# Kernel optimization log

Measured on AMD Instinct MI355X. Metric: run time of the kernel, lower is better.

Reference implementation:

```python
import jax, jax.numpy as jnp
import numpy as np
from jax import lax

DS = 4  # downsample_factor

def setup_inputs() -> dict:
    key = jax.random.key(0)
    ks = jax.random.split(key, 7)
    B, C, H, W = 4, 256, 256, 256
    Cq = C // 16  # reduction=16
    return {
        "x":  jax.random.normal(ks[0], (B, C, H, W), dtype=jnp.float32),
        "Wq": jax.random.normal(ks[1], (Cq, C), dtype=jnp.float32) * 0.05,
        "bq": jax.random.normal(ks[2], (Cq,), dtype=jnp.float32) * 0.05,
        "Wk": jax.random.normal(ks[3], (Cq, C), dtype=jnp.float32) * 0.05,
        "bk": jax.random.normal(ks[4], (Cq,), dtype=jnp.float32) * 0.05,
        "Wv": jax.random.normal(ks[5], (C, C), dtype=jnp.float32) * 0.05,
        "bv": jax.random.normal(ks[6], (C,), dtype=jnp.float32) * 0.05,
    }

def reference(x, Wq, bq, Wk, bk, Wv, bv):
    B, C, H, W = x.shape
    # MaxPool2d(kernel=DS, stride=DS)
    xd = lax.reduce_window(x, -jnp.inf, lax.max,
                           (1, 1, DS, DS), (1, 1, DS, DS), 'VALID')
    h, w = xd.shape[2], xd.shape[3]
    N = h * w
    # 1x1 convs == channel-wise linear maps
    q = jnp.einsum('oc,bchw->bohw', Wq, xd) + bq[None, :, None, None]
    k = jnp.einsum('oc,bchw->bohw', Wk, xd) + bk[None, :, None, None]
    v = jnp.einsum('oc,bchw->bohw', Wv, xd) + bv[None, :, None, None]
    query = q.reshape(B, -1, N).transpose(0, 2, 1)   # [B, N, Cq]
    key_  = k.reshape(B, -1, N)                      # [B, Cq, N]
    value = v.reshape(B, C, N).transpose(0, 2, 1)    # [B, N, C]
    att = jnp.einsum('bnc,bcm->bnm', query, key_)    # [B, N, N]
    # global-mean threshold masking (zeros, not -inf, per original)
    att = jnp.where(att < att.mean(), 0.0, att)
    att = jax.nn.softmax(att, axis=-1)
    out = jnp.einsum('bnm,bmc->bnc', att, value)     # [B, N, C]
    out = out.transpose(0, 2, 1).reshape(B, C, h, w)
    # bilinear upsample, align_corners=False (half-pixel centers)
    out = jax.image.resize(out, (B, C, H, W), method='bilinear')
    return out + x
```

## Files before the change

### kernel.cpp

```cpp
#include <hip/hip_runtime.h>
#include <hip/hip_bf16.h>
#include <cmath>
#include <cstdint>
#include <cstddef>

typedef unsigned short u16;
typedef __attribute__((ext_vector_type(8))) __bf16 bf16x8;
typedef __attribute__((ext_vector_type(4))) float f32x4;
typedef __attribute__((ext_vector_type(8))) unsigned short us8;
typedef __attribute__((ext_vector_type(4))) unsigned short us4;

static const size_t OFF_ODS   = 0;
static const size_t OFF_QT    = 16777216;
static const size_t OFF_KT    = 17825792;
static const size_t OFF_VT    = 18874368;
static const size_t OFF_SPART = 27262976;
static const size_t OFF_MEAN  = 27295744;

__device__ __forceinline__ void gl2lds16(const void* gsrc, void* ldst) {
  __builtin_amdgcn_global_load_lds(
      (const __attribute__((address_space(1))) unsigned int*)gsrc,
      (__attribute__((address_space(3))) unsigned int*)ldst, 16, 0, 0);
}

__global__ __launch_bounds__(512) void k_front(const float* __restrict__ x,
                                               const float* __restrict__ Wq, const float* __restrict__ bq,
                                               const float* __restrict__ Wk, const float* __restrict__ bk,
                                               const float* __restrict__ Wv, const float* __restrict__ bv,
                                               float* __restrict__ qT, float* __restrict__ kT,
                                               u16* __restrict__ vT, float* __restrict__ Spart) {
  __shared__ float smem[17408];
  float (*xs)[64] = reinterpret_cast<float(*)[64]>(smem);
  float (*part)[64][33] = reinterpret_cast<float(*)[64][33]>(smem);
  float (*red)[32] = reinterpret_cast<float(*)[32]>(smem + 16896);
  const int b = blockIdx.x >> 6, yo = blockIdx.x & 63;
  const int n0 = yo * 64;
  const int tid = threadIdx.x;

  {
    const float* src = x + (size_t)b * 16777216u + (size_t)(4 * yo) * 256u;
#pragma unroll
    for (int i = 0; i < 32; ++i) {
      int u = i * 512 + tid;
      int c = u >> 6, xo = u & 63;
      const float* p0 = src + (size_t)c * 65536u + xo * 4;
      float m = -1e30f;
#pragma unroll
      for (int r = 0; r < 4; ++r) {
        float4 v4 = *reinterpret_cast<const float4*>(p0 + r * 256);
        m = fmaxf(m, fmaxf(fmaxf(v4.x, v4.y), fmaxf(v4.z, v4.w)));
      }
      xs[c][xo] = m;
    }
  }
  __syncthreads();

  {
    const int ci = tid >> 4, ni = tid & 15;
    float vacc[8][4];
#pragma unroll
    for (int j = 0; j < 8; ++j) { vacc[j][0]=0.f; vacc[j][1]=0.f; vacc[j][2]=0.f; vacc[j][3]=0.f; }
    for (int cc4 = 0; cc4 < 64; ++cc4) {
      float4 xv0 = *reinterpret_cast<const float4*>(&xs[cc4*4+0][ni*4]);
      float4 xv1 = *reinterpret_cast<const float4*>(&xs[cc4*4+1][ni*4]);
      float4 xv2 = *reinterpret_cast<const float4*>(&xs[cc4*4+2][ni*4]);
      float4 xv3 = *reinterpret_cast<const float4*>(&xs[cc4*4+3][ni*4]);
#pragma unroll
      for (int j = 0; j < 8; ++j) {
        float4 wv = *reinterpret_cast<const float4*>(&Wv[(size_t)(ci*8 + j) * 256u + cc4*4]);
        vacc[j][0] = fmaf(wv.x, xv0.x, fmaf(wv.y, xv1.x, fmaf(wv.z, xv2.x, fmaf(wv.w, xv3.x, vacc[j][0]))));
        vacc[j][1] = fmaf(wv.x, xv0.y, fmaf(wv.y, xv1.y, fmaf(wv.z, xv2.y, fmaf(wv.w, xv3.y, vacc[j][1]))));
        vacc[j][2] = fmaf(wv.x, xv0.z, fmaf(wv.y, xv1.z, fmaf(wv.z, xv2.z, fmaf(wv.w, xv3.z, vacc[j][2]))));
        vacc[j][3] = fmaf(wv.x, xv0.w, fmaf(wv.y, xv1.w, fmaf(wv.z, xv2.w, fmaf(wv.w, xv3.w, vacc[j][3]))));
      }
    }
#pragma unroll
    for (int j = 0; j < 8; ++j) {
      int c = ci*8 + j;
      float bb = bv[c];
      us4 u;
#pragma unroll
      for (int nn = 0; nn < 4; ++nn)
        u[nn] = __builtin_bit_cast(u16, __float2bfloat16(vacc[j][nn] + bb));
      *reinterpret_cast<us4*>(vT + ((size_t)b*256 + c) * 4096u + n0 + ni*4) = u;
    }
  }

  const int nl = tid & 63, pp = tid >> 6;
  float qa[16], ka[16];
#pragma unroll
  for (int o = 0; o < 16; ++o) { qa[o] = 0.f; ka[o] = 0.f; }
  for (int i = 0; i < 32; ++i) {
    int c = pp * 32 + i;
    float xv = xs[c][nl];
#pragma unroll
    for (int o = 0; o < 16; ++o) {
      qa[o] = fmaf(Wq[o * 256 + c], xv, qa[o]);
      ka[o] = fmaf(Wk[o * 256 + c], xv, ka[o]);
    }
  }
  __syncthreads();
#pragma unroll
  for (int o = 0; o < 16; ++o) {
    part[pp][nl][o]      = qa[o];
    part[pp][nl][16 + o] = ka[o];
  }
  __syncthreads();
#pragma unroll
  for (int i = 0; i < 4; ++i) {
    int idx = tid * 4 + i;
    int n = idx >> 5, o = idx & 31;
    float s = 0.f;
#pragma unroll
    for (int p = 0; p < 8; ++p) s += part[p][n][o];
    if (o < 16) qT[((size_t)b * 4096u + n0 + n) * 16u + o]        = s + bq[o];
    else        kT[((size_t)b * 4096u + n0 + n) * 16u + (o - 16)] = s + bk[o - 16];
  }
  {
    int o = tid & 31, grp = tid >> 5;
    float s = 0.f;
#pragma unroll
    for (int nn = 0; nn < 4; ++nn) {
      int n = grp * 4 + nn;
#pragma unroll
      for (int p = 0; p < 8; ++p) s += part[p][n][o];
    }
    red[grp][o] = s;
  }
  __syncthreads();
  if (tid < 32) {
    float s = 0.f;
#pragma unroll
    for (int g = 0; g < 16; ++g) s += red[g][tid];
    Spart[(size_t)blockIdx.x * 32u + tid] = s;
  }
}

__global__ __launch_bounds__(64) void k_mean(const float* __restrict__ Spart,
                                             const float* __restrict__ bq, const float* __restrict__ bk,
                                             float* __restrict__ meanp) {
  int t = threadIdx.x;
  int b = t >> 4, o = t & 15;
  float sq = 4096.0f * bq[o], sk = 4096.0f * bk[o];
  for (int blk = 0; blk < 64; ++blk) {
    const float* p = Spart + ((size_t)(b * 64 + blk)) * 32u;
    sq += p[o];
    sk += p[16 + o];
  }
  float pr = sq * sk;
#pragma unroll
  for (int off = 32; off > 0; off >>= 1) pr += __shfl_down(pr, off);
  if (t == 0) *meanp = pr * (1.0f / 67108864.0f);
}

__global__ __launch_bounds__(512) void k_flash(const float* __restrict__ qT,
                                               const float* __restrict__ kT,
                                               const u16* __restrict__ vT,
                                               const float* __restrict__ meanp,
                                               float* __restrict__ ods) {
  __shared__ u16 vbuf[2][16384];
  __shared__ u16 kfh[2][4][64][8];
  __shared__ u16 kfl[2][4][64][8];
  __shared__ u16 pfr[8][2][64][8];

  const int orig = blockIdx.x;
  const int b    = (orig >> 1) & 3;
  const int row0 = (((orig & 1) << 5) | (orig >> 3)) * 64;
  const int tid  = threadIdx.x;
  const int w    = tid >> 6;
  const int lane = tid & 63;
  const int wq   = w & 3;
  const int wc   = w >> 2;
  const int g    = lane >> 4;
  const int c16  = lane & 15;

  const float mean = *meanp;

  float qv[16];
  {
    const float* qrow = qT + ((size_t)b*4096 + row0 + 16*wq + c16) * 16;
#pragma unroll
    for (int i = 0; i < 4; ++i) {
      float4 t4 = reinterpret_cast<const float4*>(qrow)[i];
      qv[4*i] = t4.x; qv[4*i+1] = t4.y; qv[4*i+2] = t4.z; qv[4*i+3] = t4.w;
    }
  }
  u16 qhi[16], qlo[16];
#pragma unroll
  for (int i = 0; i < 16; ++i) {
    __hip_bfloat16 h = __float2bfloat16(qv[i]);
    float fh = __bfloat162float(h);
    __hip_bfloat16 lo = __float2bfloat16(qv[i] - fh);
    qhi[i] = __builtin_bit_cast(u16, h);
    qlo[i] = __builtin_bit_cast(u16, lo);
  }
  us8 a1u, a2u;
  {
    const bool koff8  = (g & 1);
    const bool lo_src = (g >= 2);
#pragma unroll
    for (int i = 0; i < 8; ++i) {
      u16 hs = koff8 ? qhi[i+8] : qhi[i];
      u16 ls = koff8 ? qlo[i+8] : qlo[i];
      a1u[i] = lo_src ? ls : hs;
      a2u[i] = lo_src ? (u16)0 : hs;
    }
  }
  const bf16x8 A1 = __builtin_bit_cast(bf16x8, a1u);
  const bf16x8 A2 = __builtin_bit_cast(bf16x8, a2u);

  f32x4 O[8];
#pragma unroll
  for (int i = 0; i < 8; ++i) O[i] = (f32x4){0.f, 0.f, 0.f, 0.f};
  float Lr[4] = {0.f, 0.f, 0.f, 0.f};
  float M = 0.0f;

  const int kv_s = tid >> 2, t4v = tid & 3;
  const int ks = kv_s >> 4, kld0 = (kv_s & 15) + 16*(t4v >> 1), ki0 = 4*(t4v & 1);

  {
    const u16* vsrc = vT + (size_t)b*256*4096;
#pragma unroll
    for (int i = 0; i < 4; ++i) {
      int u = i*512 + tid;
      int row = u >> 3, slot = u & 7;
      int sb = (slot*16) ^ ((row & 7) << 4);
      gl2lds16((const char*)(vsrc + (size_t)row*4096) + sb, (char*)&vbuf[0][0] + u*16);
    }
    if (tid < 256) {
      float4 kvec = *reinterpret_cast<const float4*>(kT + ((size_t)b*4096 + kv_s)*16 + 4*t4v);
      float kf[4] = {kvec.x, kvec.y, kvec.z, kvec.w};
      us4 h4, l4;
#pragma unroll
      for (int di = 0; di < 4; ++di) {
        __hip_bfloat16 h = __float2bfloat16(kf[di]);
        float fh = __bfloat162float(h);
        __hip_bfloat16 lo = __float2bfloat16(kf[di] - fh);
        h4[di] = __builtin_bit_cast(u16, h);
        l4[di] = __builtin_bit_cast(u16, lo);
      }
      *reinterpret_cast<us4*>(&kfh[0][ks][kld0][ki0])    = h4;
      *reinterpret_cast<us4*>(&kfh[0][ks][kld0+32][ki0]) = h4;
      *reinterpret_cast<us4*>(&kfl[0][ks][kld0][ki0])    = l4;
      *reinterpret_cast<us4*>(&kfl[0][ks][kld0+32][ki0]) = l4;
    }
  }
  __syncthreads();

  for (int t = 0; t < 64; ++t) {
    const int cur = t & 1, nxt = cur ^ 1;
    const int kv0n = ((t + 1) & 63) * 64;

    float4 kvec;
    if (tid < 256)
      kvec = *reinterpret_cast<const float4*>(kT + ((size_t)b*4096 + kv0n + kv_s)*16 + 4*t4v);
    {
      const u16* vsrc = vT + (size_t)b*256*4096 + kv0n;
#pragma unroll
      for (int i = 0; i < 4; ++i) {
        int u = i*512 + tid;
        int row = u >> 3, slot = u & 7;
        int sb = (slot*16) ^ ((row & 7) << 4);
        gl2lds16((const char*)(vsrc + (size_t)row*4096) + sb, (char*)&vbuf[nxt][0] + u*16);
      }
    }

    f32x4 S[4];
#pragma unroll
    for (int s = 0; s < 4; ++s) {
      bf16x8 bh = __builtin_bit_cast(bf16x8, *reinterpret_cast<const us8*>(&kfh[cur][s][lane][0]));
      bf16x8 bl = __builtin_bit_cast(bf16x8, *reinterpret_cast<const us8*>(&kfl[cur][s][lane][0]));
      f32x4 acc = (f32x4){0.f, 0.f, 0.f, 0.f};
      acc = __builtin_amdgcn_mfma_f32_16x16x32_bf16(A1, bh, acc, 0, 0, 0);
      acc = __builtin_amdgcn_mfma_f32_16x16x32_bf16(A2, bl, acc, 0, 0, 0);
      S[s] = acc;
    }

    float pmax = -1e30f;
#pragma unroll
    for (int s = 0; s < 4; ++s)
#pragma unroll
      for (int r = 0; r < 4; ++r) {
        float v = S[s][r];
        v = (v < mean) ? 0.f : v;
        S[s][r] = v;
        pmax = fmaxf(pmax, v);
      }
    if (!__all(pmax <= M + 8.0f)) {
      float mw = pmax;
#pragma unroll
      for (int off = 1; off < 64; off <<= 1) mw = fmaxf(mw, __shfl_xor(mw, off));
      float Mn = fmaxf(M, mw);
      float sc = __expf(M - Mn);
#pragma unroll
      for (int i = 0; i < 8; ++i) {
        O[i][0] *= sc; O[i][1] *= sc; O[i][2] *= sc; O[i][3] *= sc;
      }
#pragma unroll
      for (int r = 0; r < 4; ++r) Lr[r] *= sc;
      M = Mn;
    }
    u16 pb[4][4];
#pragma unroll
    for (int s = 0; s < 4; ++s)
#pragma unroll
      for (int r = 0; r < 4; ++r) {
        float p = __expf(S[s][r] - M);
        Lr[r] += p;
        pb[s][r] = __builtin_bit_cast(u16, __float2bfloat16(p));
      }

    {
      const int ib = lane & 7;
      const int t1 = (lane >> 3) & 1;
#pragma unroll
      for (int s = 0; s < 4; ++s) {
        const int c2 = s >> 1;
        const int ldb = 16 * ((2*s + t1) & 3) + 4*g;
#pragma unroll
        for (int r = 0; r < 4; ++r) pfr[w][c2][ldb + r][ib] = pb[s][r];
      }
    }
    asm volatile("s_waitcnt lgkmcnt(0)" ::: "memory");
    __builtin_amdgcn_sched_barrier(0);

#pragma unroll
    for (int c2 = 0; c2 < 2; ++c2) {
      bf16x8 pa = __builtin_bit_cast(bf16x8, *reinterpret_cast<const us8*>(&pfr[w][c2][lane][0]));
#pragma unroll
      for (int ct = 0; ct < 8; ++ct) {
        int row = (wc*8 + ct)*16 + c16;
        int off = (c2*64 + g*16) ^ ((lane & 7) << 4);
        bf16x8 vb = __builtin_bit_cast(bf16x8,
            *reinterpret_cast<const us8*>((const char*)&vbuf[cur][0] + row*128 + off));
        O[ct] = __builtin_amdgcn_mfma_f32_16x16x32_bf16(pa, vb, O[ct], 0, 0, 0);
      }
    }

    if (tid < 256) {
      float kf[4] = {kvec.x, kvec.y, kvec.z, kvec.w};
      us4 h4, l4;
#pragma unroll
      for (int di = 0; di < 4; ++di) {
        __hip_bfloat16 h = __float2bfloat16(kf[di]);
        float fh = __bfloat162float(h);
        __hip_bfloat16 lo = __float2bfloat16(kf[di] - fh);
        h4[di] = __builtin_bit_cast(u16, h);
        l4[di] = __builtin_bit_cast(u16, lo);
      }
      *reinterpret_cast<us4*>(&kfh[nxt][ks][kld0][ki0])    = h4;
      *reinterpret_cast<us4*>(&kfh[nxt][ks][kld0+32][ki0]) = h4;
      *reinterpret_cast<us4*>(&kfl[nxt][ks][kld0][ki0])    = l4;
      *reinterpret_cast<us4*>(&kfl[nxt][ks][kld0+32][ki0]) = l4;
    }

    __syncthreads();
  }

#pragma unroll
  for (int r = 0; r < 4; ++r) {
    float v = Lr[r];
#pragma unroll
    for (int off = 1; off < 16; off <<= 1) v += __shfl_xor(v, off);
    Lr[r] = v;
  }
  float inv[4];
#pragma unroll
  for (int r = 0; r < 4; ++r) inv[r] = 1.0f / Lr[r];
#pragma unroll
  for (int ct = 0; ct < 8; ++ct) {
    int c = (wc*8 + ct)*16 + c16;
    float* dst = ods + ((size_t)b*256 + c) * 4096u + row0 + 16*wq + 4*g;
    float4 o4 = make_float4(O[ct][0]*inv[0], O[ct][1]*inv[1], O[ct][2]*inv[2], O[ct][3]*inv[3]);
    *reinterpret_cast<float4*>(dst) = o4;
  }
}

__global__ __launch_bounds__(256) void k_up(const float* __restrict__ ods, const float* __restrict__ x,
                                            float* __restrict__ out) {
  unsigned idx4 = blockIdx.x * 256u + threadIdx.x;
  int a  = (int)(idx4 & 63u);
  int i  = (int)((idx4 >> 6) & 255u);
  size_t bc = idx4 >> 14;

  float py = (i + 0.5f) * 0.25f - 0.5f;
  float y0f = floorf(py);
  float wy = py - y0f;
  int y0 = (int)y0f, y1 = y0 + 1;
  y0 = max(y0, 0); y1 = min(y1, 63);

  int xm1 = max(a - 1, 0), xp1 = min(a + 1, 63);

  const float* r0 = ods + bc * 4096u + y0 * 64;
  const float* r1 = ods + bc * 4096u + y1 * 64;
  float wy1 = 1.f - wy;
  float vm1 = wy1 * r0[xm1] + wy * r1[xm1];
  float v0  = wy1 * r0[a]   + wy * r1[a];
  float vp1 = wy1 * r0[xp1] + wy * r1[xp1];

  float4 xv = *reinterpret_cast<const float4*>(x + (size_t)idx4 * 4u);
  float4 o4;
  o4.x = fmaf(0.375f, vm1, 0.625f * v0) + xv.x;
  o4.y = fmaf(0.125f, vm1, 0.875f * v0) + xv.y;
  o4.z = fmaf(0.875f, v0, 0.125f * vp1) + xv.z;
  o4.w = fmaf(0.625f, v0, 0.375f * vp1) + xv.w;
  *reinterpret_cast<float4*>(out + (size_t)idx4 * 4u) = o4;
}

extern "C" void kernel_launch(void* const* d_in, const int* in_sizes, int n_in,
                              void* d_out, int out_size, void* d_ws, size_t ws_size,
                              hipStream_t stream) {
  const float* x  = (const float*)d_in[0];
  const float* Wq = (const float*)d_in[1];
  const float* bq = (const float*)d_in[2];
  const float* Wk = (const float*)d_in[3];
  const float* bk = (const float*)d_in[4];
  const float* Wv = (const float*)d_in[5];
  const float* bv = (const float*)d_in[6];
  float* out = (float*)d_out;

  char* ws = (char*)d_ws;
  float* ods   = (float*)(ws + OFF_ODS);
  float* qT    = (float*)(ws + OFF_QT);
  float* kT    = (float*)(ws + OFF_KT);
  u16*   vT    = (u16*)(ws + OFF_VT);
  float* Spart = (float*)(ws + OFF_SPART);
  float* mnp   = (float*)(ws + OFF_MEAN);

  k_front<<<dim3(256), dim3(512), 0, stream>>>(x, Wq, bq, Wk, bk, Wv, bv, qT, kT, vT, Spart);
  k_mean<<<dim3(1), dim3(64), 0, stream>>>(Spart, bq, bk, mnp);
  k_flash<<<dim3(256), dim3(512), 0, stream>>>(qT, kT, vT, mnp, ods);
  k_up<<<dim3(65536), dim3(256), 0, stream>>>(ods, x, out);
}
```

Before: 297.7 us.

## Split max-pool out of front kernel into a massively parallel pooling kernel

Moves the 4x4 max-pool out of the 256-block front kernel into its own kernel with 16384 blocks, so the full read of x uses the whole GPU instead of being limited to 256 large blocks. The pooled tensor is written to workspace (reusing the ods buffer) and the QKV kernel then loads it with coalesced float4 reads. This adds a kernel launch and an extra write and read of the small pooled tensor.

Result: slower. 310.4 us (+4.3%).

```diff
diff --git a/kernel.cpp b/kernel.cpp
--- a/kernel.cpp
+++ b/kernel.cpp
@@ -23,34 +23,43 @@
       (__attribute__((address_space(3))) unsigned int*)ldst, 16, 0, 0);
 }
 
-__global__ __launch_bounds__(512) void k_front(const float* __restrict__ x,
-                                               const float* __restrict__ Wq, const float* __restrict__ bq,
-                                               const float* __restrict__ Wk, const float* __restrict__ bk,
-                                               const float* __restrict__ Wv, const float* __restrict__ bv,
-                                               float* __restrict__ qT, float* __restrict__ kT,
-                                               u16* __restrict__ vT, float* __restrict__ Spart) {
+__global__ __launch_bounds__(256) void k_pool(const float* __restrict__ x,
+                                              float* __restrict__ xd) {
+  unsigned idx = blockIdx.x * 256u + threadIdx.x;
+  unsigned xo = idx & 63u;
+  unsigned yo = (idx >> 6) & 63u;
+  unsigned bc = idx >> 12;
+  const float* base = x + (size_t)bc * 65536u + yo * 1024u + xo * 4u;
+  float m = -1e30f;
+#pragma unroll
+  for (int dy = 0; dy < 4; ++dy) {
+    float4 v = *reinterpret_cast<const float4*>(base + dy * 256);
+    m = fmaxf(m, fmaxf(fmaxf(v.x, v.y), fmaxf(v.z, v.w)));
+  }
+  xd[(size_t)bc * 4096u + yo * 64u + xo] = m;
+}
+
+__global__ __launch_bounds__(512) void k_qkv(const float* __restrict__ xd,
+                                             const float* __restrict__ Wq, const float* __restrict__ bq,
+                                             const float* __restrict__ Wk, const float* __restrict__ bk,
+                                             const float* __restrict__ Wv, const float* __restrict__ bv,
+                                             float* __restrict__ qT, float* __restrict__ kT,
+                                             u16* __restrict__ vT, float* __restrict__ Spart) {
   __shared__ float smem[17408];
   float (*xs)[64] = reinterpret_cast<float(*)[64]>(smem);
   float (*part)[64][33] = reinterpret_cast<float(*)[64][33]>(smem);
   float (*red)[32] = reinterpret_cast<float(*)[32]>(smem + 16896);
-  const int b = blockIdx.x >> 6, yo = blockIdx.x & 63;
-  const int n0 = yo * 64;
+  const int b = blockIdx.x >> 6, n0 = (blockIdx.x & 63) * 64;
   const int tid = threadIdx.x;
 
   {
-    const float* src = x + (size_t)b * 16777216u + (size_t)(4 * yo) * 256u;
-#pragma unroll
-    for (int i = 0; i < 32; ++i) {
-      int u = i * 512 + tid;
-      int c = u >> 6, xo = u & 63;
-      const float* p0 = src + (size_t)c * 65536u + xo * 4;
-      float m = -1e30f;
-#pragma unroll
-      for (int r = 0; r < 4; ++r) {
-        float4 v4 = *reinterpret_cast<const float4*>(p0 + r * 256);
-        m = fmaxf(m, fmaxf(fmaxf(v4.x, v4.y), fmaxf(v4.z, v4.w)));
-      }
-      xs[c][xo] = m;
+    const float* src = xd + (size_t)b * 1048576u + n0;
+#pragma unroll
+    for (int i = 0; i < 8; ++i) {
+      int l4 = tid + i * 512;
+      int c = l4 >> 4, qq = l4 & 15;
+      *reinterpret_cast<float4*>(&xs[c][qq * 4]) =
+          *reinterpret_cast<const float4*>(src + (size_t)c * 4096u + qq * 4);
     }
   }
   __syncthreads();
@@ -420,14 +429,16 @@
   float* out = (float*)d_out;
 
   char* ws = (char*)d_ws;
-  float* ods   = (float*)(ws + OFF_ODS);
+  float* xd    = (float*)(ws + OFF_ODS);
   float* qT    = (float*)(ws + OFF_QT);
   float* kT    = (float*)(ws + OFF_KT);
   u16*   vT    = (u16*)(ws + OFF_VT);
   float* Spart = (float*)(ws + OFF_SPART);
   float* mnp   = (float*)(ws + OFF_MEAN);
-
-  k_front<<<dim3(256), dim3(512), 0, stream>>>(x, Wq, bq, Wk, bk, Wv, bv, qT, kT, vT, Spart);
+  float* ods   = xd;
+
+  k_pool<<<dim3(16384), dim3(256), 0, stream>>>(x, xd);
+  k_qkv<<<dim3(256), dim3(512), 0, stream>>>(xd, Wq, bq, Wk, bk, Wv, bv, qT, kT, vT, Spart);
   k_mean<<<dim3(1), dim3(64), 0, stream>>>(Spart, bq, bk, mnp);
   k_flash<<<dim3(256), dim3(512), 0, stream>>>(qT, kT, vT, mnp, ods);
   k_up<<<dim3(65536), dim3(256), 0, stream>>>(ods, x, out);
```

## Split front kernel into 1024 smaller blocks of 16 tokens each

Applied to the files above, without the earlier changes.

The pooling and projection kernel now launches 1024 blocks of 256 threads, each handling a quarter of a pooled row (16 tokens), instead of 256 blocks of 512 threads. This fills more compute units during the memory-bound max-pool phase. The q/k projection now reduces across lanes with shuffles, and the V projection assigns one output channel per thread. The cost is that Wv and Wq/Wk are re-read by four times as many blocks, and the mean kernel must sum four times as many partials.

Result: slower. 344.9 us (+15.8%).

```diff
diff --git a/kernel.cpp b/kernel.cpp
--- a/kernel.cpp
+++ b/kernel.cpp
@@ -15,7 +15,7 @@
 static const size_t OFF_KT    = 17825792;
 static const size_t OFF_VT    = 18874368;
 static const size_t OFF_SPART = 27262976;
-static const size_t OFF_MEAN  = 27295744;
+static const size_t OFF_MEAN  = 27394048;
 
 __device__ __forceinline__ void gl2lds16(const void* gsrc, void* ldst) {
   __builtin_amdgcn_global_load_lds(
@@ -23,116 +23,134 @@
       (__attribute__((address_space(3))) unsigned int*)ldst, 16, 0, 0);
 }
 
-__global__ __launch_bounds__(512) void k_front(const float* __restrict__ x,
+__device__ __forceinline__ float hmax4(float4 v) {
+  return fmaxf(fmaxf(v.x, v.y), fmaxf(v.z, v.w));
+}
+
+__global__ __launch_bounds__(256) void k_front(const float* __restrict__ x,
                                                const float* __restrict__ Wq, const float* __restrict__ bq,
                                                const float* __restrict__ Wk, const float* __restrict__ bk,
                                                const float* __restrict__ Wv, const float* __restrict__ bv,
                                                float* __restrict__ qT, float* __restrict__ kT,
                                                u16* __restrict__ vT, float* __restrict__ Spart) {
-  __shared__ float smem[17408];
-  float (*xs)[64] = reinterpret_cast<float(*)[64]>(smem);
-  float (*part)[64][33] = reinterpret_cast<float(*)[64][33]>(smem);
-  float (*red)[32] = reinterpret_cast<float(*)[32]>(smem + 16896);
-  const int b = blockIdx.x >> 6, yo = blockIdx.x & 63;
-  const int n0 = yo * 64;
+  __shared__ float xs[256][20];
+  __shared__ float part2[4][16][33];
+  const int blk = blockIdx.x;
+  const int b   = blk >> 8;
+  const int yo  = (blk >> 2) & 63;
+  const int qtr = blk & 3;
+  const int n0  = yo * 64 + qtr * 16;
   const int tid = threadIdx.x;
 
   {
-    const float* src = x + (size_t)b * 16777216u + (size_t)(4 * yo) * 256u;
-#pragma unroll
-    for (int i = 0; i < 32; ++i) {
-      int u = i * 512 + tid;
-      int c = u >> 6, xo = u & 63;
-      const float* p0 = src + (size_t)c * 65536u + xo * 4;
-      float m = -1e30f;
+    const int jc = tid & 3;
+    const int crow = tid >> 2;
+    const float* base = x + (size_t)b * 16777216u + (size_t)(4 * yo) * 256u + qtr * 64 + jc * 16;
+#pragma unroll
+    for (int ci = 0; ci < 4; ++ci) {
+      int c = ci * 64 + crow;
+      const float* pc = base + (size_t)c * 65536u;
+      float m0 = -1e30f, m1 = -1e30f, m2 = -1e30f, m3 = -1e30f;
 #pragma unroll
       for (int r = 0; r < 4; ++r) {
-        float4 v4 = *reinterpret_cast<const float4*>(p0 + r * 256);
-        m = fmaxf(m, fmaxf(fmaxf(v4.x, v4.y), fmaxf(v4.z, v4.w)));
-      }
-      xs[c][xo] = m;
+        const float4* row = reinterpret_cast<const float4*>(pc + r * 256);
+        m0 = fmaxf(m0, hmax4(row[0]));
+        m1 = fmaxf(m1, hmax4(row[1]));
+        m2 = fmaxf(m2, hmax4(row[2]));
+        m3 = fmaxf(m3, hmax4(row[3]));
+      }
+      *reinterpret_cast<float4*>(&xs[c][jc * 4]) = make_float4(m0, m1, m2, m3);
     }
   }
   __syncthreads();
 
   {
-    const int ci = tid >> 4, ni = tid & 15;
-    float vacc[8][4];
-#pragma unroll
-    for (int j = 0; j < 8; ++j) { vacc[j][0]=0.f; vacc[j][1]=0.f; vacc[j][2]=0.f; vacc[j][3]=0.f; }
-    for (int cc4 = 0; cc4 < 64; ++cc4) {
-      float4 xv0 = *reinterpret_cast<const float4*>(&xs[cc4*4+0][ni*4]);
-      float4 xv1 = *reinterpret_cast<const float4*>(&xs[cc4*4+1][ni*4]);
-      float4 xv2 = *reinterpret_cast<const float4*>(&xs[cc4*4+2][ni*4]);
-      float4 xv3 = *reinterpret_cast<const float4*>(&xs[cc4*4+3][ni*4]);
-#pragma unroll
-      for (int j = 0; j < 8; ++j) {
-        float4 wv = *reinterpret_cast<const float4*>(&Wv[(size_t)(ci*8 + j) * 256u + cc4*4]);
-        vacc[j][0] = fmaf(wv.x, xv0.x, fmaf(wv.y, xv1.x, fmaf(wv.z, xv2.x, fmaf(wv.w, xv3.x, vacc[j][0]))));
-        vacc[j][1] = fmaf(wv.x, xv0.y, fmaf(wv.y, xv1.y, fmaf(wv.z, xv2.y, fmaf(wv.w, xv3.y, vacc[j][1]))));
-        vacc[j][2] = fmaf(wv.x, xv0.z, fmaf(wv.y, xv1.z, fmaf(wv.z, xv2.z, fmaf(wv.w, xv3.z, vacc[j][2]))));
-        vacc[j][3] = fmaf(wv.x, xv0.w, fmaf(wv.y, xv1.w, fmaf(wv.z, xv2.w, fmaf(wv.w, xv3.w, vacc[j][3]))));
-      }
-    }
-#pragma unroll
-    for (int j = 0; j < 8; ++j) {
-      int c = ci*8 + j;
-      float bb = bv[c];
-      us4 u;
-#pragma unroll
-      for (int nn = 0; nn < 4; ++nn)
-        u[nn] = __builtin_bit_cast(u16, __float2bfloat16(vacc[j][nn] + bb));
-      *reinterpret_cast<us4*>(vT + ((size_t)b*256 + c) * 4096u + n0 + ni*4) = u;
-    }
-  }
-
-  const int nl = tid & 63, pp = tid >> 6;
-  float qa[16], ka[16];
-#pragma unroll
-  for (int o = 0; o < 16; ++o) { qa[o] = 0.f; ka[o] = 0.f; }
-  for (int i = 0; i < 32; ++i) {
-    int c = pp * 32 + i;
-    float xv = xs[c][nl];
+    const int cg = tid >> 4, tok = tid & 15;
+    float qac[16], kac[16];
+#pragma unroll
+    for (int o = 0; o < 16; ++o) { qac[o] = 0.f; kac[o] = 0.f; }
+#pragma unroll
+    for (int i4 = 0; i4 < 4; ++i4) {
+      float xv0 = xs[cg * 16 + i4 * 4 + 0][tok];
+      float xv1 = xs[cg * 16 + i4 * 4 + 1][tok];
+      float xv2 = xs[cg * 16 + i4 * 4 + 2][tok];
+      float xv3 = xs[cg * 16 + i4 * 4 + 3][tok];
+#pragma unroll
+      for (int o = 0; o < 16; ++o) {
+        float4 q4 = *reinterpret_cast<const float4*>(&Wq[o * 256 + cg * 16 + i4 * 4]);
+        float4 k4 = *reinterpret_cast<const float4*>(&Wk[o * 256 + cg * 16 + i4 * 4]);
+        qac[o] = fmaf(q4.x, xv0, fmaf(q4.y, xv1, fmaf(q4.z, xv2, fmaf(q4.w, xv3, qac[o]))));
+        kac[o] = fmaf(k4.x, xv0, fmaf(k4.y, xv1, fmaf(k4.z, xv2, fmaf(k4.w, xv3, kac[o]))));
+      }
+    }
 #pragma unroll
     for (int o = 0; o < 16; ++o) {
-      qa[o] = fmaf(Wq[o * 256 + c], xv, qa[o]);
-      ka[o] = fmaf(Wk[o * 256 + c], xv, ka[o]);
+      qac[o] += __shfl_xor(qac[o], 16); qac[o] += __shfl_xor(qac[o], 32);
+      kac[o] += __shfl_xor(kac[o], 16); kac[o] += __shfl_xor(kac[o], 32);
+    }
+    const int w = tid >> 6, lane = tid & 63;
+    if (lane < 16) {
+#pragma unroll
+      for (int o = 0; o < 16; ++o) {
+        part2[w][lane][o]      = qac[o];
+        part2[w][lane][16 + o] = kac[o];
+      }
     }
   }
   __syncthreads();
-#pragma unroll
-  for (int o = 0; o < 16; ++o) {
-    part[pp][nl][o]      = qa[o];
-    part[pp][nl][16 + o] = ka[o];
-  }
-  __syncthreads();
-#pragma unroll
-  for (int i = 0; i < 4; ++i) {
-    int idx = tid * 4 + i;
-    int n = idx >> 5, o = idx & 31;
-    float s = 0.f;
-#pragma unroll
-    for (int p = 0; p < 8; ++p) s += part[p][n][o];
-    if (o < 16) qT[((size_t)b * 4096u + n0 + n) * 16u + o]        = s + bq[o];
-    else        kT[((size_t)b * 4096u + n0 + n) * 16u + (o - 16)] = s + bk[o - 16];
-  }
-  {
-    int o = tid & 31, grp = tid >> 5;
-    float s = 0.f;
-#pragma unroll
-    for (int nn = 0; nn < 4; ++nn) {
-      int n = grp * 4 + nn;
-#pragma unroll
-      for (int p = 0; p < 8; ++p) s += part[p][n][o];
-    }
-    red[grp][o] = s;
-  }
-  __syncthreads();
+
+#pragma unroll
+  for (int j = 0; j < 2; ++j) {
+    int idx = tid + j * 256;
+    int tt = idx >> 5, o = idx & 31;
+    float s = part2[0][tt][o] + part2[1][tt][o] + part2[2][tt][o] + part2[3][tt][o];
+    if (o < 16) qT[((size_t)b * 4096u + n0 + tt) * 16u + o]        = s + bq[o];
+    else        kT[((size_t)b * 4096u + n0 + tt) * 16u + (o - 16)] = s + bk[o - 16];
+  }
   if (tid < 32) {
     float s = 0.f;
 #pragma unroll
-    for (int g = 0; g < 16; ++g) s += red[g][tid];
-    Spart[(size_t)blockIdx.x * 32u + tid] = s;
+    for (int tt = 0; tt < 16; ++tt)
+#pragma unroll
+      for (int w = 0; w < 4; ++w) s += part2[w][tt][tid];
+    Spart[(size_t)blk * 32u + tid] = s;
+  }
+
+  {
+    float acc[16];
+#pragma unroll
+    for (int i = 0; i < 16; ++i) acc[i] = 0.f;
+    const float* wrow = Wv + (size_t)tid * 256u;
+    for (int kk = 0; kk < 64; ++kk) {
+      float4 wv = *reinterpret_cast<const float4*>(&wrow[kk * 4]);
+#pragma unroll
+      for (int u = 0; u < 4; ++u) {
+        int k = kk * 4 + u;
+        float ws = (u == 0) ? wv.x : (u == 1) ? wv.y : (u == 2) ? wv.z : wv.w;
+        float4 x0 = *reinterpret_cast<const float4*>(&xs[k][0]);
+        float4 x1 = *reinterpret_cast<const float4*>(&xs[k][4]);
+        float4 x2 = *reinterpret_cast<const float4*>(&xs[k][8]);
+        float4 x3 = *reinterpret_cast<const float4*>(&xs[k][12]);
+        acc[0]  = fmaf(ws, x0.x, acc[0]);  acc[1]  = fmaf(ws, x0.y, acc[1]);
+        acc[2]  = fmaf(ws, x0.z, acc[2]);  acc[3]  = fmaf(ws, x0.w, acc[3]);
+        acc[4]  = fmaf(ws, x1.x, acc[4]);  acc[5]  = fmaf(ws, x1.y, acc[5]);
+        acc[6]  = fmaf(ws, x1.z, acc[6]);  acc[7]  = fmaf(ws, x1.w, acc[7]);
+        acc[8]  = fmaf(ws, x2.x, acc[8]);  acc[9]  = fmaf(ws, x2.y, acc[9]);
+        acc[10] = fmaf(ws, x2.z, acc[10]); acc[11] = fmaf(ws, x2.w, acc[11]);
+        acc[12] = fmaf(ws, x3.x, acc[12]); acc[13] = fmaf(ws, x3.y, acc[13]);
+        acc[14] = fmaf(ws, x3.z, acc[14]); acc[15] = fmaf(ws, x3.w, acc[15]);
+      }
+    }
+    float bb = bv[tid];
+    u16* dst = vT + ((size_t)b * 256u + tid) * 4096u + n0;
+    us8 o0, o1;
+#pragma unroll
+    for (int i = 0; i < 8; ++i) {
+      o0[i] = __builtin_bit_cast(u16, __float2bfloat16(acc[i] + bb));
+      o1[i] = __builtin_bit_cast(u16, __float2bfloat16(acc[8 + i] + bb));
+    }
+    *reinterpret_cast<us8*>(dst)     = o0;
+    *reinterpret_cast<us8*>(dst + 8) = o1;
   }
 }
 
@@ -142,8 +160,8 @@
   int t = threadIdx.x;
   int b = t >> 4, o = t & 15;
   float sq = 4096.0f * bq[o], sk = 4096.0f * bk[o];
-  for (int blk = 0; blk < 64; ++blk) {
-    const float* p = Spart + ((size_t)(b * 64 + blk)) * 32u;
+  for (int blk = 0; blk < 256; ++blk) {
+    const float* p = Spart + ((size_t)(b * 256 + blk)) * 32u;
     sq += p[o];
     sk += p[16 + o];
   }
@@ -427,7 +445,7 @@
   float* Spart = (float*)(ws + OFF_SPART);
   float* mnp   = (float*)(ws + OFF_MEAN);
 
-  k_front<<<dim3(256), dim3(512), 0, stream>>>(x, Wq, bq, Wk, bk, Wv, bv, qT, kT, vT, Spart);
+  k_front<<<dim3(1024), dim3(256), 0, stream>>>(x, Wq, bq, Wk, bk, Wv, bv, qT, kT, vT, Spart);
   k_mean<<<dim3(1), dim3(64), 0, stream>>>(Spart, bq, bk, mnp);
   k_flash<<<dim3(256), dim3(512), 0, stream>>>(qT, kT, vT, mnp, ods);
   k_up<<<dim3(65536), dim3(256), 0, stream>>>(ods, x, out);
```
